# Optimization experiments

Measured on AMD Instinct MI355X. Metric: run time of the kernel, lower is better.

## Reference

```python
import jax, jax.numpy as jnp
import numpy as np
from jax import lax

H = 64          # GRU hidden size
OUT_STEPS = 20  # output_seq_size


def _maxpool2(x):
    # x: [N, C, H, W] -> 2x2 max pool, stride 2, VALID
    return lax.reduce_window(x, -jnp.inf, lax.max, (1, 1, 2, 2), (1, 1, 2, 2), 'VALID')


def _conv(x, w, b):
    # NCHW / OIHW, VALID, stride 1
    y = lax.conv_general_dilated(x, w, (1, 1), 'VALID',
                                 dimension_numbers=('NCHW', 'OIHW', 'NCHW'))
    return y + b[None, :, None, None]


def _gru_step(h, x, wih, whh, bih, bhh):
    # PyTorch GRU gate order: r, z, n
    gi = x @ wih.T + bih            # [B, 3H]
    gh = h @ whh.T + bhh            # [B, 3H]
    i_r, i_z, i_n = jnp.split(gi, 3, axis=-1)
    h_r, h_z, h_n = jnp.split(gh, 3, axis=-1)
    r = jax.nn.sigmoid(i_r + h_r)
    z = jax.nn.sigmoid(i_z + h_z)
    n = jnp.tanh(i_n + r * h_n)
    return (1.0 - z) * n + z * h


def setup_inputs() -> dict:
    key = jax.random.key(0)
    ks = jax.random.split(key, 20)
    B, T = 1024, 31
    s = 0.1
    return {
        'bbox_seq': jax.random.normal(ks[0], (B, T, 4), jnp.float32),
        'head_seq': jax.random.uniform(ks[1], (B, T, 32, 32), jnp.float32),
        'conv1_w': jax.random.normal(ks[2], (4, 1, 3, 3), jnp.float32) * s,
        'conv1_b': jax.random.normal(ks[3], (4,), jnp.float32) * s,
        'conv2_w': jax.random.normal(ks[4], (10, 4, 3, 3), jnp.float32) * s,
        'conv2_b': jax.random.normal(ks[5], (10,), jnp.float32) * s,
        'fc_w': jax.random.normal(ks[6], (5, 360), jnp.float32) * s,
        'fc_b': jax.random.normal(ks[7], (5,), jnp.float32) * s,
        'enc_wih': jax.random.normal(ks[8], (3 * H, 9), jnp.float32) * s,
        'enc_whh': jax.random.normal(ks[9], (3 * H, H), jnp.float32) * s,
        'enc_bih': jax.random.normal(ks[10], (3 * H,), jnp.float32) * s,
        'enc_bhh': jax.random.normal(ks[11], (3 * H,), jnp.float32) * s,
        'dec_wih': jax.random.normal(ks[12], (3 * H, 4), jnp.float32) * s,
        'dec_whh': jax.random.normal(ks[13], (3 * H, H), jnp.float32) * s,
        'dec_bih': jax.random.normal(ks[14], (3 * H,), jnp.float32) * s,
        'dec_bhh': jax.random.normal(ks[15], (3 * H,), jnp.float32) * s,
        'lin_w': jax.random.normal(ks[16], (4, H), jnp.float32) * s,
        'lin_b': jax.random.normal(ks[17], (4,), jnp.float32) * s,
    }


def reference(bbox_seq, head_seq, conv1_w, conv1_b, conv2_w, conv2_b, fc_w, fc_b,
              enc_wih, enc_whh, enc_bih, enc_bhh,
              dec_wih, dec_whh, dec_bih, dec_bhh, lin_w, lin_b):
    B, T = bbox_seq.shape[0], bbox_seq.shape[1]
    L = T - 1  # encoder sequence length

    # offset: last bbox, broadcast over OUT_STEPS -> [B, OUT_STEPS, 4]
    offset = jnp.broadcast_to(bbox_seq[:, -1][:, None, :], (B, OUT_STEPS, 4))

    diffs = bbox_seq[:, 1:] - bbox_seq[:, :-1]  # [B, L, 4] (dropout p=0 -> identity)

    # --- ConvEncoder on all head crops at once ---
    imgs = head_seq[:, :-1].reshape(B * L, 1, 32, 32)
    x = jax.nn.relu(_conv(imgs, conv1_w, conv1_b))   # [BL, 4, 30, 30]
    x = _maxpool2(x)                                  # [BL, 4, 15, 15]
    x = jax.nn.relu(_conv(x, conv2_w, conv2_b))       # [BL, 10, 13, 13]
    x = _maxpool2(x)                                  # [BL, 10, 6, 6]
    emb = x.reshape(B * L, -1) @ fc_w.T + fc_b        # [BL, 5]
    emb = emb.reshape(B, L, -1)

    enc_in = jnp.concatenate([diffs, emb], axis=2)    # [B, L, 9]

    # --- GRU encoder (scan over time) ---
    def enc_step(h, x_t):
        h = _gru_step(h, x_t, enc_wih, enc_whh, enc_bih, enc_bhh)
        return h, None
    h0 = jnp.zeros((B, H), enc_in.dtype)
    hn, _ = lax.scan(enc_step, h0, jnp.swapaxes(enc_in, 0, 1))

    def dec_step(carry, _):
        h, prev_x = carry
        h = _gru_step(h, prev_x, dec_wih, dec_whh, dec_bih, dec_bhh)
        x_new = h @ lin_w.T + lin_b + prev_x
        return (h, x_new), x_new
    (_, _), outs = lax.scan(dec_step, (hn, diffs[:, -1]), None, length=OUT_STEPS)
    out = jnp.swapaxes(outs, 0, 1)                    # [B, OUT_STEPS, 4]

    return jnp.cumsum(out, axis=1) + offset
```

## Files before the change

### kernel.cpp

```cpp
#include <hip/hip_runtime.h>
#include <hip/hip_bf16.h>


#define B_    1024
#define L_    30
#define H_    64

typedef _Float16 half_t;
typedef __attribute__((ext_vector_type(2))) _Float16 half2_t;

__device__ __forceinline__ float sigmoid_f(float v) {
    return 1.f / (1.f + __expf(-v));
}
__device__ __forceinline__ float tanh_f(float v) {
    v = fminf(fmaxf(v, -15.f), 15.f);
    float e = __expf(2.f * v);
    return (e - 1.f) / (e + 1.f);
}
__device__ __forceinline__ void load4_lds(float* r, const float* p) {
    float2 a = *(const float2*)p;
    float2 b = *(const float2*)(p + 2);
    r[0] = a.x; r[1] = a.y; r[2] = b.x; r[3] = b.y;
}

__global__ __launch_bounds__(64) void conv_embed_kernel(
    const float* __restrict__ bbox,
    const float* __restrict__ head,
    const float* __restrict__ c1w, const float* __restrict__ c1b,
    const float* __restrict__ c2w, const float* __restrict__ c2b,
    const float* __restrict__ fcw, const float* __restrict__ fcb,
    float* __restrict__ enc_in)
{
    const int img = blockIdx.x;
    const int b = img / L_;
    const int l = img % L_;
    const int tid = threadIdx.x;

    __shared__ float s_img[32 * 32];
    __shared__ float s_p1[4 * 15 * 16];
    __shared__ float s_p2[360];
    __shared__ float s_red[60];

    {
        const float4* src = (const float4*)(head + ((size_t)b * 31 + (size_t)l) * 1024);
        float4* dst = (float4*)s_img;
        #pragma unroll
        for (int i = 0; i < 4; ++i) dst[tid + 64 * i] = src[tid + 64 * i];
    }
    __syncthreads();

    if (tid < 60) {
        const int c = tid / 15, px = tid % 15;
        const int x0 = 2 * px;
        float wg[9];
        #pragma unroll
        for (int k = 0; k < 9; ++k) wg[k] = c1w[c * 9 + k];
        const float bias = c1b[c];

        auto c1out = [&](const float* ra, const float* rb, const float* rc, const float* rd) -> float {
            float a00 = bias, a01 = bias, a10 = bias, a11 = bias;
            #pragma unroll
            for (int kx = 0; kx < 3; ++kx) {
                const float w0 = wg[kx], w1 = wg[3 + kx], w2 = wg[6 + kx];
                a00 = fmaf(w0, ra[kx],     fmaf(w1, rb[kx],     fmaf(w2, rc[kx],     a00)));
                a01 = fmaf(w0, ra[kx + 1], fmaf(w1, rb[kx + 1], fmaf(w2, rc[kx + 1], a01)));
                a10 = fmaf(w0, rb[kx],     fmaf(w1, rc[kx],     fmaf(w2, rd[kx],     a10)));
                a11 = fmaf(w0, rb[kx + 1], fmaf(w1, rc[kx + 1], fmaf(w2, rd[kx + 1], a11)));
            }
            a00 = fmaxf(a00, 0.f); a01 = fmaxf(a01, 0.f);
            a10 = fmaxf(a10, 0.f); a11 = fmaxf(a11, 0.f);
            return fmaxf(fmaxf(a00, a01), fmaxf(a10, a11));
        };

        float r[6][4];
        load4_lds(r[0], s_img + 0 * 32 + x0);
        load4_lds(r[1], s_img + 1 * 32 + x0);
        #pragma unroll
        for (int i = 0; i < 7; ++i) {
            const int s0 = (4 * i) % 6, s1 = (4 * i + 1) % 6, s2 = (4 * i + 2) % 6;
            const int s3 = (4 * i + 3) % 6, s4 = (4 * i + 4) % 6, s5 = (4 * i + 5) % 6;
            load4_lds(r[s2], s_img + (4 * i + 2) * 32 + x0);
            load4_lds(r[s3], s_img + (4 * i + 3) * 32 + x0);
            s_p1[c * 240 + (2 * i) * 16 + px] = c1out(r[s0], r[s1], r[s2], r[s3]);
            load4_lds(r[s4], s_img + (4 * i + 4) * 32 + x0);
            load4_lds(r[s5], s_img + (4 * i + 5) * 32 + x0);
            s_p1[c * 240 + (2 * i + 1) * 16 + px] = c1out(r[s2], r[s3], r[s4], r[s5]);
        }
        load4_lds(r[0], s_img + 30 * 32 + x0);
        load4_lds(r[1], s_img + 31 * 32 + x0);
        s_p1[c * 240 + 14 * 16 + px] = c1out(r[4], r[5], r[0], r[1]);
    }
    __syncthreads();

    if (tid < 60) {
        const int c = tid / 6, px = tid % 6;
        const int x0 = 2 * px;
        float wg2[4][9];
        #pragma unroll
        for (int ic = 0; ic < 4; ++ic)
            #pragma unroll
            for (int k = 0; k < 9; ++k) wg2[ic][k] = c2w[(c * 4 + ic) * 9 + k];
        const float bias2 = c2b[c];

        float P[6][4][4];
        auto c2out = [&](float (*pa)[4], float (*pb)[4], float (*pc)[4], float (*pd)[4]) -> float {
            float a00 = bias2, a01 = bias2, a10 = bias2, a11 = bias2;
            #pragma unroll
            for (int ic = 0; ic < 4; ++ic) {
                #pragma unroll
                for (int kx = 0; kx < 3; ++kx) {
                    const float w0 = wg2[ic][kx], w1 = wg2[ic][3 + kx], w2 = wg2[ic][6 + kx];
                    a00 = fmaf(w0, pa[ic][kx],     fmaf(w1, pb[ic][kx],     fmaf(w2, pc[ic][kx],     a00)));
                    a01 = fmaf(w0, pa[ic][kx + 1], fmaf(w1, pb[ic][kx + 1], fmaf(w2, pc[ic][kx + 1], a01)));
                    a10 = fmaf(w0, pb[ic][kx],     fmaf(w1, pc[ic][kx],     fmaf(w2, pd[ic][kx],     a10)));
                    a11 = fmaf(w0, pb[ic][kx + 1], fmaf(w1, pc[ic][kx + 1], fmaf(w2, pd[ic][kx + 1], a11)));
                }
            }
            a00 = fmaxf(a00, 0.f); a01 = fmaxf(a01, 0.f);
            a10 = fmaxf(a10, 0.f); a11 = fmaxf(a11, 0.f);
            return fmaxf(fmaxf(a00, a01), fmaxf(a10, a11));
        };

        #pragma unroll
        for (int ic = 0; ic < 4; ++ic) {
            load4_lds(P[0][ic], s_p1 + ic * 240 + 0 * 16 + x0);
            load4_lds(P[1][ic], s_p1 + ic * 240 + 1 * 16 + x0);
        }
        #pragma unroll
        for (int i = 0; i < 3; ++i) {
            const int s0 = (4 * i) % 6, s1 = (4 * i + 1) % 6, s2 = (4 * i + 2) % 6;
            const int s3 = (4 * i + 3) % 6, s4 = (4 * i + 4) % 6, s5 = (4 * i + 5) % 6;
            #pragma unroll
            for (int ic = 0; ic < 4; ++ic) {
                load4_lds(P[s2][ic], s_p1 + ic * 240 + (4 * i + 2) * 16 + x0);
                load4_lds(P[s3][ic], s_p1 + ic * 240 + (4 * i + 3) * 16 + x0);
            }
            s_p2[c * 36 + (2 * i) * 6 + px] = c2out(P[s0], P[s1], P[s2], P[s3]);
            #pragma unroll
            for (int ic = 0; ic < 4; ++ic) {
                load4_lds(P[s4][ic], s_p1 + ic * 240 + (4 * i + 4) * 16 + x0);
                load4_lds(P[s5][ic], s_p1 + ic * 240 + (4 * i + 5) * 16 + x0);
            }
            s_p2[c * 36 + (2 * i + 1) * 6 + px] = c2out(P[s2], P[s3], P[s4], P[s5]);
        }
    }
    __syncthreads();

    if (tid < 60) {
        const int o = tid / 12, i0 = tid % 12;
        const float* wrow = fcw + o * 360;
        float acc = 0.f;
        #pragma unroll
        for (int k = 0; k < 30; ++k) {
            const int i = i0 + 12 * k;
            acc = fmaf(wrow[i], s_p2[i], acc);
        }
        s_red[tid] = acc;
    }
    __syncthreads();

    float* dst = enc_in + ((size_t)b * L_ + l) * 9;
    if (tid < 5) {
        float acc = fcb[tid];
        #pragma unroll
        for (int k = 0; k < 12; ++k) acc += s_red[tid * 12 + k];
        dst[4 + tid] = acc;
    } else if (tid >= 8 && tid < 12) {
        const int d = tid - 8;
        const float* bb = bbox + (size_t)b * 124 + (size_t)l * 4;
        dst[d] = bb[4 + d] - bb[d];
    }
}

__global__ __launch_bounds__(64, 1) void gru_encdec_kernel(
    const float* __restrict__ bbox,
    const float* __restrict__ enc_in,
    const float* __restrict__ ewih, const float* __restrict__ ewhh,
    const float* __restrict__ ebih, const float* __restrict__ ebhh,
    const float* __restrict__ dwih, const float* __restrict__ dwhh,
    const float* __restrict__ dbih, const float* __restrict__ dbhh,
    const float* __restrict__ linw, const float* __restrict__ linb,
    float* __restrict__ out)
{
    const int b = blockIdx.x;
    const int j = threadIdx.x;

    __shared__ float  xs[272];
    __shared__ half_t hs[64];

    for (int i = j; i < 270; i += 64) xs[i] = enc_in[(size_t)b * 270 + i];

    float h = 0.f;

    {
        half2_t Wh2[3][32];
        #pragma unroll
        for (int g = 0; g < 3; ++g) {
            const float4* row = (const float4*)(ewhh + (size_t)(g * 64 + j) * 64);
            #pragma unroll
            for (int k4 = 0; k4 < 16; ++k4) {
                const float4 v = row[k4];
                Wh2[g][2 * k4]     = half2_t{(half_t)v.x, (half_t)v.y};
                Wh2[g][2 * k4 + 1] = half2_t{(half_t)v.z, (half_t)v.w};
            }
        }
        float Wi[3][9];
        #pragma unroll
        for (int g = 0; g < 3; ++g) {
            const float* row = ewih + (g * 64 + j) * 9;
            #pragma unroll
            for (int k = 0; k < 9; ++k) Wi[g][k] = row[k];
        }
        const float bi0 = ebih[j], bi1 = ebih[64 + j], bi2 = ebih[128 + j];
        const float bh0 = ebhh[j], bh1 = ebhh[64 + j], bh2 = ebhh[128 + j];

        __syncthreads();

        #pragma unroll 1
        for (int t = 0; t < L_; ++t) {
            hs[j] = (half_t)h;
            __builtin_amdgcn_wave_barrier();

            float gr = bi0 + bh0, gz = bi1 + bh1, gni = bi2, gnh = bh2;
            #pragma unroll
            for (int k = 0; k < 9; ++k) {
                const float xk = xs[t * 9 + k];
                gr  = fmaf(Wi[0][k], xk, gr);
                gz  = fmaf(Wi[1][k], xk, gz);
                gni = fmaf(Wi[2][k], xk, gni);
            }
            const half2_t* hp = (const half2_t*)hs;
            #pragma unroll
            for (int k2 = 0; k2 < 32; ++k2) {
                const half2_t h2 = hp[k2];
                gr  = __builtin_amdgcn_fdot2(Wh2[0][k2], h2, gr,  false);
                gz  = __builtin_amdgcn_fdot2(Wh2[1][k2], h2, gz,  false);
                gnh = __builtin_amdgcn_fdot2(Wh2[2][k2], h2, gnh, false);
            }
            const float r = sigmoid_f(gr);
            const float z = sigmoid_f(gz);
            const float n = tanh_f(gni + r * gnh);
            h = (1.f - z) * n + z * h;
            __builtin_amdgcn_wave_barrier();
        }
    }

    {
        half2_t Wh2[3][32];
        #pragma unroll
        for (int g = 0; g < 3; ++g) {
            const float4* row = (const float4*)(dwhh + (size_t)(g * 64 + j) * 64);
            #pragma unroll
            for (int k4 = 0; k4 < 16; ++k4) {
                const float4 v = row[k4];
                Wh2[g][2 * k4]     = half2_t{(half_t)v.x, (half_t)v.y};
                Wh2[g][2 * k4 + 1] = half2_t{(half_t)v.z, (half_t)v.w};
            }
        }
        float Wi[3][4];
        #pragma unroll
        for (int g = 0; g < 3; ++g) {
            const float* row = dwih + (g * 64 + j) * 4;
            #pragma unroll
            for (int k = 0; k < 4; ++k) Wi[g][k] = row[k];
        }
        const float bi0 = dbih[j], bi1 = dbih[64 + j], bi2 = dbih[128 + j];
        const float bh0 = dbhh[j], bh1 = dbhh[64 + j], bh2 = dbhh[128 + j];
        const float lw0 = linw[j], lw1 = linw[64 + j], lw2 = linw[128 + j], lw3 = linw[192 + j];
        const float lb0 = linb[0], lb1 = linb[1], lb2 = linb[2], lb3 = linb[3];

        const float* bb = bbox + (size_t)b * 124;
        float px0 = bb[120] - bb[116];
        float px1 = bb[121] - bb[117];
        float px2 = bb[122] - bb[118];
        float px3 = bb[123] - bb[119];
        const float of0 = bb[120], of1 = bb[121], of2 = bb[122], of3 = bb[123];
        float cs0 = 0.f, cs1 = 0.f, cs2 = 0.f, cs3 = 0.f;
        float4* outp = (float4*)(out + (size_t)b * 80);

        #pragma unroll 1
        for (int t = 0; t < 20; ++t) {
            hs[j] = (half_t)h;
            __builtin_amdgcn_wave_barrier();

            float gr = bi0 + bh0, gz = bi1 + bh1, gni = bi2, gnh = bh2;
            gr  = fmaf(Wi[0][0], px0, fmaf(Wi[0][1], px1, fmaf(Wi[0][2], px2, fmaf(Wi[0][3], px3, gr))));
            gz  = fmaf(Wi[1][0], px0, fmaf(Wi[1][1], px1, fmaf(Wi[1][2], px2, fmaf(Wi[1][3], px3, gz))));
            gni = fmaf(Wi[2][0], px0, fmaf(Wi[2][1], px1, fmaf(Wi[2][2], px2, fmaf(Wi[2][3], px3, gni))));

            const half2_t* hp = (const half2_t*)hs;
            #pragma unroll
            for (int k2 = 0; k2 < 32; ++k2) {
                const half2_t h2 = hp[k2];
                gr  = __builtin_amdgcn_fdot2(Wh2[0][k2], h2, gr,  false);
                gz  = __builtin_amdgcn_fdot2(Wh2[1][k2], h2, gz,  false);
                gnh = __builtin_amdgcn_fdot2(Wh2[2][k2], h2, gnh, false);
            }
            const float r = sigmoid_f(gr);
            const float z = sigmoid_f(gz);
            const float n = tanh_f(gni + r * gnh);
            h = (1.f - z) * n + z * h;
            __builtin_amdgcn_wave_barrier();

            float v0 = lw0 * h, v1 = lw1 * h, v2 = lw2 * h, v3 = lw3 * h;
            #pragma unroll
            for (int s = 32; s > 0; s >>= 1) {
                v0 += __shfl_xor(v0, s);
                v1 += __shfl_xor(v1, s);
                v2 += __shfl_xor(v2, s);
                v3 += __shfl_xor(v3, s);
            }
            px0 = v0 + lb0 + px0;
            px1 = v1 + lb1 + px1;
            px2 = v2 + lb2 + px2;
            px3 = v3 + lb3 + px3;
            cs0 += px0; cs1 += px1; cs2 += px2; cs3 += px3;
            if (j == 0) outp[t] = make_float4(cs0 + of0, cs1 + of1, cs2 + of2, cs3 + of3);
        }
    }
}

extern "C" void kernel_launch(void* const* d_in, const int* in_sizes, int n_in,
                              void* d_out, int out_size, void* d_ws, size_t ws_size,
                              hipStream_t stream) {
    (void)in_sizes; (void)n_in; (void)out_size; (void)ws_size;
    const float* bbox = (const float*)d_in[0];
    const float* head = (const float*)d_in[1];
    const float* c1w  = (const float*)d_in[2];
    const float* c1b  = (const float*)d_in[3];
    const float* c2w  = (const float*)d_in[4];
    const float* c2b  = (const float*)d_in[5];
    const float* fcw  = (const float*)d_in[6];
    const float* fcb  = (const float*)d_in[7];
    const float* ewih = (const float*)d_in[8];
    const float* ewhh = (const float*)d_in[9];
    const float* ebih = (const float*)d_in[10];
    const float* ebhh = (const float*)d_in[11];
    const float* dwih = (const float*)d_in[12];
    const float* dwhh = (const float*)d_in[13];
    const float* dbih = (const float*)d_in[14];
    const float* dbhh = (const float*)d_in[15];
    const float* linw = (const float*)d_in[16];
    const float* linb = (const float*)d_in[17];
    float* out = (float*)d_out;

    float* enc_in = (float*)d_ws;

    conv_embed_kernel<<<B_ * L_, 64, 0, stream>>>(bbox, head, c1w, c1b, c2w, c2b,
                                                  fcw, fcb, enc_in);
    gru_encdec_kernel<<<B_, 64, 0, stream>>>(bbox, enc_in,
                                             ewih, ewhh, ebih, ebhh,
                                             dwih, dwhh, dbih, dbhh,
                                             linw, linb, out);
}
```

Before: 298.3 us.

## Rewrite GRU encoder/decoder with MFMA batching 16 sequences per block

```diff
diff --git a/kernel.cpp b/kernel.cpp
--- a/kernel.cpp
+++ b/kernel.cpp
@@ -7,15 +7,18 @@
 #define H_    64
 
 typedef _Float16 half_t;
-typedef __attribute__((ext_vector_type(2))) _Float16 half2_t;
+typedef __attribute__((ext_vector_type(8))) _Float16 half8;
+typedef __attribute__((ext_vector_type(4))) float f32x4;
+
+#define MFMA16(A, B, C) __builtin_amdgcn_mfma_f32_16x16x32_f16(A, B, C, 0, 0, 0)
 
 __device__ __forceinline__ float sigmoid_f(float v) {
-    return 1.f / (1.f + __expf(-v));
+    return __builtin_amdgcn_rcpf(1.f + __expf(-v));
 }
 __device__ __forceinline__ float tanh_f(float v) {
     v = fminf(fmaxf(v, -15.f), 15.f);
-    float e = __expf(2.f * v);
-    return (e - 1.f) / (e + 1.f);
+    const float e = __expf(2.f * v);
+    return (e - 1.f) * __builtin_amdgcn_rcpf(e + 1.f);
 }
 __device__ __forceinline__ void load4_lds(float* r, const float* p) {
     float2 a = *(const float2*)p;
@@ -172,7 +175,7 @@
     }
 }
 
-__global__ __launch_bounds__(64, 1) void gru_encdec_kernel(
+__global__ __launch_bounds__(256, 1) void gru_mfma_kernel(
     const float* __restrict__ bbox,
     const float* __restrict__ enc_in,
     const float* __restrict__ ewih, const float* __restrict__ ewhh,
@@ -182,141 +185,167 @@
     const float* __restrict__ linw, const float* __restrict__ linb,
     float* __restrict__ out)
 {
-    const int b = blockIdx.x;
-    const int j = threadIdx.x;
-
-    __shared__ float  xs[272];
-    __shared__ half_t hs[64];
-
-    for (int i = j; i < 270; i += 64) xs[i] = enc_in[(size_t)b * 270 + i];
-
-    float h = 0.f;
+    const int bb  = blockIdx.x * 16;
+    const int tid = threadIdx.x;
+    const int w   = tid >> 6;
+    const int l   = tid & 63;
+    const int q   = l >> 4;
+    const int col = l & 15;
+
+    alignas(16) __shared__ half_t hbuf[2][16][72];
+    alignas(16) __shared__ half_t xenc[30][16][40];
+    alignas(16) __shared__ half_t xdec[16][40];
 
     {
-        half2_t Wh2[3][32];
-        #pragma unroll
-        for (int g = 0; g < 3; ++g) {
-            const float4* row = (const float4*)(ewhh + (size_t)(g * 64 + j) * 64);
-            #pragma unroll
-            for (int k4 = 0; k4 < 16; ++k4) {
-                const float4 v = row[k4];
-                Wh2[g][2 * k4]     = half2_t{(half_t)v.x, (half_t)v.y};
-                Wh2[g][2 * k4 + 1] = half2_t{(half_t)v.z, (half_t)v.w};
-            }
-        }
-        float Wi[3][9];
-        #pragma unroll
-        for (int g = 0; g < 3; ++g) {
-            const float* row = ewih + (g * 64 + j) * 9;
-            #pragma unroll
-            for (int k = 0; k < 9; ++k) Wi[g][k] = row[k];
-        }
-        const float bi0 = ebih[j], bi1 = ebih[64 + j], bi2 = ebih[128 + j];
-        const float bh0 = ebhh[j], bh1 = ebhh[64 + j], bh2 = ebhh[128 + j];
-
+        int4* p = (int4*)hbuf;
+        for (int i = tid; i < (int)(sizeof(hbuf) / 16); i += 256) p[i] = int4{0, 0, 0, 0};
+        p = (int4*)xenc;
+        for (int i = tid; i < (int)(sizeof(xenc) / 16); i += 256) p[i] = int4{0, 0, 0, 0};
+        p = (int4*)xdec;
+        for (int i = tid; i < (int)(sizeof(xdec) / 16); i += 256) p[i] = int4{0, 0, 0, 0};
+    }
+    __syncthreads();
+
+    for (int pr = tid; pr < 480; pr += 256) {
+        const int t = pr / 16, b = pr % 16;
+        const float* src = enc_in + ((size_t)(bb + b) * L_ + t) * 9;
+        #pragma unroll
+        for (int d = 0; d < 9; ++d) xenc[t][b][d] = (half_t)src[d];
+    }
+
+    float xold[4], ofs[4], cs[4];
+    if (w == 0 && col < 4) {
+        #pragma unroll
+        for (int r = 0; r < 4; ++r) {
+            const float* bbp = bbox + (size_t)(bb + q * 4 + r) * 124;
+            xold[r] = bbp[120 + col] - bbp[116 + col];
+            ofs[r]  = bbp[120 + col];
+            cs[r]   = 0.f;
+            xdec[q * 4 + r][col] = (half_t)xold[r];
+        }
+    }
+
+    const int urow = 16 * w + col;
+    auto whh_frag = [&](const float* W, int gate, int kap) -> half8 {
+        const float* rp = W + (size_t)(gate * 64 + urow) * 64 + kap * 32 + q * 8;
+        half8 f;
+        #pragma unroll
+        for (int j = 0; j < 8; ++j) f[j] = (half_t)rp[j];
+        return f;
+    };
+    auto wih_frag = [&](const float* W, int gate, int indim) -> half8 {
+        half8 f;
+        #pragma unroll
+        for (int j = 0; j < 8; ++j) {
+            const int d = q * 8 + j;
+            f[j] = (d < indim) ? (half_t)W[(size_t)(gate * 64 + urow) * indim + d]
+                               : (half_t)0.f;
+        }
+        return f;
+    };
+
+    const half8 eBr0 = whh_frag(ewhh, 0, 0), eBr1 = whh_frag(ewhh, 0, 1);
+    const half8 eBz0 = whh_frag(ewhh, 1, 0), eBz1 = whh_frag(ewhh, 1, 1);
+    const half8 eBn0 = whh_frag(ewhh, 2, 0), eBn1 = whh_frag(ewhh, 2, 1);
+    const half8 eBrx = wih_frag(ewih, 0, 9);
+    const half8 eBzx = wih_frag(ewih, 1, 9);
+    const half8 eBnx = wih_frag(ewih, 2, 9);
+
+    const half8 dBr0 = whh_frag(dwhh, 0, 0), dBr1 = whh_frag(dwhh, 0, 1);
+    const half8 dBz0 = whh_frag(dwhh, 1, 0), dBz1 = whh_frag(dwhh, 1, 1);
+    const half8 dBn0 = whh_frag(dwhh, 2, 0), dBn1 = whh_frag(dwhh, 2, 1);
+    const half8 dBrx = wih_frag(dwih, 0, 4);
+    const half8 dBzx = wih_frag(dwih, 1, 4);
+    const half8 dBnx = wih_frag(dwih, 2, 4);
+
+    half8 Bl0, Bl1;
+    #pragma unroll
+    for (int j = 0; j < 8; ++j) {
+        Bl0[j] = (col < 4) ? (half_t)linw[col * 64 +      q * 8 + j] : (half_t)0.f;
+        Bl1[j] = (col < 4) ? (half_t)linw[col * 64 + 32 + q * 8 + j] : (half_t)0.f;
+    }
+
+    const float ebr  = ebih[urow]       + ebhh[urow];
+    const float ebz  = ebih[64 + urow]  + ebhh[64 + urow];
+    const float ebnh = ebhh[128 + urow];
+    const float ebni = ebih[128 + urow];
+    const float dbr  = dbih[urow]       + dbhh[urow];
+    const float dbz  = dbih[64 + urow]  + dbhh[64 + urow];
+    const float dbnh = dbhh[128 + urow];
+    const float dbni = dbih[128 + urow];
+    const float lb   = (col < 4) ? linb[col] : 0.f;
+
+    float hold[4] = {0.f, 0.f, 0.f, 0.f};
+    __syncthreads();
+
+    for (int t = 0; t < L_; ++t) {
+        const int p = t & 1;
+        const half8 a0 = *(const half8*)&hbuf[p][col][q * 8];
+        const half8 a1 = *(const half8*)&hbuf[p][col][32 + q * 8];
+        const half8 a2 = *(const half8*)&xenc[t][col][q * 8];
+
+        f32x4 Cr  = {ebr, ebr, ebr, ebr};
+        f32x4 Cz  = {ebz, ebz, ebz, ebz};
+        f32x4 Cnh = {ebnh, ebnh, ebnh, ebnh};
+        f32x4 Cnx = {ebni, ebni, ebni, ebni};
+        Cr  = MFMA16(a0, eBr0, Cr);  Cr  = MFMA16(a1, eBr1, Cr);  Cr = MFMA16(a2, eBrx, Cr);
+        Cz  = MFMA16(a0, eBz0, Cz);  Cz  = MFMA16(a1, eBz1, Cz);  Cz = MFMA16(a2, eBzx, Cz);
+        Cnh = MFMA16(a0, eBn0, Cnh); Cnh = MFMA16(a1, eBn1, Cnh);
+        Cnx = MFMA16(a2, eBnx, Cnx);
+
+        #pragma unroll
+        for (int r = 0; r < 4; ++r) {
+            const float rr = sigmoid_f(Cr[r]);
+            const float zz = sigmoid_f(Cz[r]);
+            const float nn = tanh_f(Cnx[r] + rr * Cnh[r]);
+            hold[r] = fmaf(zz, hold[r] - nn, nn);
+            hbuf[p ^ 1][q * 4 + r][urow] = (half_t)hold[r];
+        }
         __syncthreads();
-
-        #pragma unroll 1
-        for (int t = 0; t < L_; ++t) {
-            hs[j] = (half_t)h;
-            __builtin_amdgcn_wave_barrier();
-
-            float gr = bi0 + bh0, gz = bi1 + bh1, gni = bi2, gnh = bh2;
-            #pragma unroll
-            for (int k = 0; k < 9; ++k) {
-                const float xk = xs[t * 9 + k];
-                gr  = fmaf(Wi[0][k], xk, gr);
-                gz  = fmaf(Wi[1][k], xk, gz);
-                gni = fmaf(Wi[2][k], xk, gni);
-            }
-            const half2_t* hp = (const half2_t*)hs;
-            #pragma unroll
-            for (int k2 = 0; k2 < 32; ++k2) {
-                const half2_t h2 = hp[k2];
-                gr  = __builtin_amdgcn_fdot2(Wh2[0][k2], h2, gr,  false);
-                gz  = __builtin_amdgcn_fdot2(Wh2[1][k2], h2, gz,  false);
-                gnh = __builtin_amdgcn_fdot2(Wh2[2][k2], h2, gnh, false);
-            }
-            const float r = sigmoid_f(gr);
-            const float z = sigmoid_f(gz);
-            const float n = tanh_f(gni + r * gnh);
-            h = (1.f - z) * n + z * h;
-            __builtin_amdgcn_wave_barrier();
-        }
-    }
-
-    {
-        half2_t Wh2[3][32];
-        #pragma unroll
-        for (int g = 0; g < 3; ++g) {
-            const float4* row = (const float4*)(dwhh + (size_t)(g * 64 + j) * 64);
-            #pragma unroll
-            for (int k4 = 0; k4 < 16; ++k4) {
-                const float4 v = row[k4];
-                Wh2[g][2 * k4]     = half2_t{(half_t)v.x, (half_t)v.y};
-                Wh2[g][2 * k4 + 1] = half2_t{(half_t)v.z, (half_t)v.w};
-            }
-        }
-        float Wi[3][4];
-        #pragma unroll
-        for (int g = 0; g < 3; ++g) {
-            const float* row = dwih + (g * 64 + j) * 4;
-            #pragma unroll
-            for (int k = 0; k < 4; ++k) Wi[g][k] = row[k];
-        }
-        const float bi0 = dbih[j], bi1 = dbih[64 + j], bi2 = dbih[128 + j];
-        const float bh0 = dbhh[j], bh1 = dbhh[64 + j], bh2 = dbhh[128 + j];
-        const float lw0 = linw[j], lw1 = linw[64 + j], lw2 = linw[128 + j], lw3 = linw[192 + j];
-        const float lb0 = linb[0], lb1 = linb[1], lb2 = linb[2], lb3 = linb[3];
-
-        const float* bb = bbox + (size_t)b * 124;
-        float px0 = bb[120] - bb[116];
-        float px1 = bb[121] - bb[117];
-        float px2 = bb[122] - bb[118];
-        float px3 = bb[123] - bb[119];
-        const float of0 = bb[120], of1 = bb[121], of2 = bb[122], of3 = bb[123];
-        float cs0 = 0.f, cs1 = 0.f, cs2 = 0.f, cs3 = 0.f;
-        float4* outp = (float4*)(out + (size_t)b * 80);
-
-        #pragma unroll 1
-        for (int t = 0; t < 20; ++t) {
-            hs[j] = (half_t)h;
-            __builtin_amdgcn_wave_barrier();
-
-            float gr = bi0 + bh0, gz = bi1 + bh1, gni = bi2, gnh = bh2;
-            gr  = fmaf(Wi[0][0], px0, fmaf(Wi[0][1], px1, fmaf(Wi[0][2], px2, fmaf(Wi[0][3], px3, gr))));
-            gz  = fmaf(Wi[1][0], px0, fmaf(Wi[1][1], px1, fmaf(Wi[1][2], px2, fmaf(Wi[1][3], px3, gz))));
-            gni = fmaf(Wi[2][0], px0, fmaf(Wi[2][1], px1, fmaf(Wi[2][2], px2, fmaf(Wi[2][3], px3, gni))));
-
-            const half2_t* hp = (const half2_t*)hs;
-            #pragma unroll
-            for (int k2 = 0; k2 < 32; ++k2) {
-                const half2_t h2 = hp[k2];
-                gr  = __builtin_amdgcn_fdot2(Wh2[0][k2], h2, gr,  false);
-                gz  = __builtin_amdgcn_fdot2(Wh2[1][k2], h2, gz,  false);
-                gnh = __builtin_amdgcn_fdot2(Wh2[2][k2], h2, gnh, false);
-            }
-            const float r = sigmoid_f(gr);
-            const float z = sigmoid_f(gz);
-            const float n = tanh_f(gni + r * gnh);
-            h = (1.f - z) * n + z * h;
-            __builtin_amdgcn_wave_barrier();
-
-            float v0 = lw0 * h, v1 = lw1 * h, v2 = lw2 * h, v3 = lw3 * h;
-            #pragma unroll
-            for (int s = 32; s > 0; s >>= 1) {
-                v0 += __shfl_xor(v0, s);
-                v1 += __shfl_xor(v1, s);
-                v2 += __shfl_xor(v2, s);
-                v3 += __shfl_xor(v3, s);
-            }
-            px0 = v0 + lb0 + px0;
-            px1 = v1 + lb1 + px1;
-            px2 = v2 + lb2 + px2;
-            px3 = v3 + lb3 + px3;
-            cs0 += px0; cs1 += px1; cs2 += px2; cs3 += px3;
-            if (j == 0) outp[t] = make_float4(cs0 + of0, cs1 + of1, cs2 + of2, cs3 + of3);
-        }
+    }
+
+    for (int tt = 0; tt < 20; ++tt) {
+        const int p = tt & 1;
+        const half8 a0 = *(const half8*)&hbuf[p][col][q * 8];
+        const half8 a1 = *(const half8*)&hbuf[p][col][32 + q * 8];
+        const half8 a2 = *(const half8*)&xdec[col][q * 8];
+
+        f32x4 Cr  = {dbr, dbr, dbr, dbr};
+        f32x4 Cz  = {dbz, dbz, dbz, dbz};
+        f32x4 Cnh = {dbnh, dbnh, dbnh, dbnh};
+        f32x4 Cnx = {dbni, dbni, dbni, dbni};
+        Cr  = MFMA16(a0, dBr0, Cr);  Cr  = MFMA16(a1, dBr1, Cr);  Cr = MFMA16(a2, dBrx, Cr);
+        Cz  = MFMA16(a0, dBz0, Cz);  Cz  = MFMA16(a1, dBz1, Cz);  Cz = MFMA16(a2, dBzx, Cz);
+        Cnh = MFMA16(a0, dBn0, Cnh); Cnh = MFMA16(a1, dBn1, Cnh);
+        Cnx = MFMA16(a2, dBnx, Cnx);
+
+        #pragma unroll
+        for (int r = 0; r < 4; ++r) {
+            const float rr = sigmoid_f(Cr[r]);
+            const float zz = sigmoid_f(Cz[r]);
+            const float nn = tanh_f(Cnx[r] + rr * Cnh[r]);
+            hold[r] = fmaf(zz, hold[r] - nn, nn);
+            hbuf[p ^ 1][q * 4 + r][urow] = (half_t)hold[r];
+        }
+        __syncthreads();
+
+        const half8 al0 = *(const half8*)&hbuf[p ^ 1][col][q * 8];
+        const half8 al1 = *(const half8*)&hbuf[p ^ 1][col][32 + q * 8];
+        f32x4 X = {0.f, 0.f, 0.f, 0.f};
+        X = MFMA16(al0, Bl0, X);
+        X = MFMA16(al1, Bl1, X);
+
+        if (w == 0 && col < 4) {
+            #pragma unroll
+            for (int r = 0; r < 4; ++r) {
+                const float xv = X[r] + lb + xold[r];
+                xold[r] = xv;
+                cs[r] += xv;
+                xdec[q * 4 + r][col] = (half_t)xv;
+                out[(size_t)(bb + q * 4 + r) * 80 + tt * 4 + col] = cs[r] + ofs[r];
+            }
+        }
+        __syncthreads();
     }
 }
 
@@ -348,8 +377,8 @@
 
     conv_embed_kernel<<<B_ * L_, 64, 0, stream>>>(bbox, head, c1w, c1b, c2w, c2b,
                                                   fcw, fcb, enc_in);
-    gru_encdec_kernel<<<B_, 64, 0, stream>>>(bbox, enc_in,
-                                             ewih, ewhh, ebih, ebhh,
-                                             dwih, dwhh, dbih, dbhh,
-                                             linw, linb, out);
-}
+    gru_mfma_kernel<<<B_ / 16, 256, 0, stream>>>(bbox, enc_in,
+                                                 ewih, ewhh, ebih, ebhh,
+                                                 dwih, dwhh, dbih, dbhh,
+                                                 linw, linb, out);
+}
```

Result: faster. 284.5 us (-4.6%).
